# Performance work log

Hardware: AMD Instinct MI355X
Metric: run time of the kernel (lower is better)

The kernel has to match this reference:

```python
import jax, jax.numpy as jnp
import numpy as np

N = 50000   # nodes
E = 800000  # edges
D = 128     # input_dim
H = 128     # hidden_dim
C = 40      # output_dim (classes)


def setup_inputs() -> dict:
    key = jax.random.key(0)
    ks = jax.random.split(key, 8)
    x = jax.random.normal(ks[0], (N, D), dtype=jnp.float32)
    edge_index = jax.random.randint(ks[1], (2, E), 0, N, dtype=jnp.int32)
    sD = 1.0 / np.sqrt(D)
    sH = 1.0 / np.sqrt(H)
    W1 = jax.random.uniform(ks[2], (D, H), jnp.float32, -sD, sD)
    b1 = jnp.zeros((H,), jnp.float32)
    W2 = jax.random.uniform(ks[3], (H, H), jnp.float32, -sH, sH)
    b2 = jnp.zeros((H,), jnp.float32)
    W3 = jax.random.uniform(ks[4], (H, C), jnp.float32, -sH, sH)
    b3 = jnp.zeros((C,), jnp.float32)
    return {"x": x, "edge_index": edge_index,
            "W1": W1, "b1": b1, "W2": W2, "b2": b2, "W3": W3, "b3": b3}


def reference(x, edge_index, W1, b1, W2, b2, W3, b3):
    # GCNConv: out = D^{-1/2} (A + I) D^{-1/2} (x @ W) + b
    src = edge_index[0]
    dst = edge_index[1]
    loop = jnp.arange(N, dtype=src.dtype)
    src_f = jnp.concatenate([src, loop])  # [E+N] with self-loops
    dst_f = jnp.concatenate([dst, loop])
    deg = jax.ops.segment_sum(jnp.ones(E + N, x.dtype), dst_f, num_segments=N)
    dinv = jax.lax.rsqrt(jnp.maximum(deg, 1.0))  # deg >= 1 due to self-loops
    norm = dinv[src_f] * dinv[dst_f]  # [E+N]

    def conv(h, W, b):
        h = h @ W                       # [N, F_out]
        msg = h[src_f] * norm[:, None]  # [E+N, F_out] gathered messages
        return jax.ops.segment_sum(msg, dst_f, num_segments=N) + b

    h = jax.nn.relu(conv(x, W1, b1))
    h = jax.nn.relu(conv(h, W2, b2))  # dropout is identity in eval mode
    return conv(h, W3, b3)
```

## Files before the change

### kernel.cpp

```cpp
#include <hip/hip_runtime.h>

typedef unsigned short ushort_t;
typedef unsigned int uint_t;


__global__ __launch_bounds__(256) void k_scan(
        const int* __restrict__ deg, unsigned long long* __restrict__ partials,
        int* __restrict__ rowptr, int* __restrict__ cursor,
        float* __restrict__ dinv, int n) {
    __shared__ int s[256];
    __shared__ int sprefix;
    const int b = blockIdx.x, t = threadIdx.x;
    const int i = b * 256 + t;
    int v = (i < n) ? deg[i] : 0;
    s[t] = v;
    __syncthreads();
    for (int off = 1; off < 256; off <<= 1) {
        int u = (t >= off) ? s[t - off] : 0;
        __syncthreads();
        s[t] += u;
        __syncthreads();
    }
    if (t == 0) {
        __hip_atomic_store(&partials[b],
                ((unsigned long long)s[255] << 2) | 1ull,
                __ATOMIC_RELEASE, __HIP_MEMORY_SCOPE_AGENT);
        if (b == 0) {
            __hip_atomic_store(&partials[0],
                    ((unsigned long long)s[255] << 2) | 2ull,
                    __ATOMIC_RELEASE, __HIP_MEMORY_SCOPE_AGENT);
            sprefix = 0;
        }
    }
    if (b > 0 && t < 64) {
        int acc = 0;
        int k = b - 1;
        for (;;) {
            int idx = k - t;
            unsigned long long p;
            unsigned st;
            do {
                if (idx >= 0) {
                    p = __hip_atomic_load(&partials[idx],
                            __ATOMIC_ACQUIRE, __HIP_MEMORY_SCOPE_AGENT);
                } else {
                    p = 2ull;
                }
                st = (unsigned)(p & 3ull);
            } while (st == 0);
            unsigned long long bal = __ballot(st == 2);
            int L = (bal != 0) ? (__ffsll((unsigned long long)bal) - 1) : 64;
            int val = (int)(p >> 2);
            int contrib = (t <= L) ? val : 0;
            #pragma unroll
            for (int o = 32; o > 0; o >>= 1) contrib += __shfl_down(contrib, o);
            if (t == 0) acc += contrib;
            if (L < 64) break;
            k -= 64;
        }
        if (t == 0) {
            __hip_atomic_store(&partials[b],
                    (((unsigned long long)(acc + s[255])) << 2) | 2ull,
                    __ATOMIC_RELEASE, __HIP_MEMORY_SCOPE_AGENT);
            sprefix = acc;
        }
    }
    __syncthreads();
    if (i < n) {
        int ex = sprefix + s[t] - v;
        rowptr[i] = ex;
        cursor[i] = ex;
        dinv[i] = rsqrtf((float)(v + 1));
        if (i == n - 1) rowptr[n] = ex + v;
    }
}

__global__ __launch_bounds__(256) void k_fill(const int* __restrict__ ei,
                                              int* __restrict__ cursor,
                                              const float* __restrict__ dinv,
                                              int2* __restrict__ csr, int E, int n) {
    const int xcd = blockIdx.x & 7;
    const int e = (blockIdx.x >> 3) * 256 + threadIdx.x;
    if (e >= E) return;
    int d = ei[E + e];
    const int lo = (int)(((long long)xcd * n) >> 3);
    const int hi = (int)(((long long)(xcd + 1) * n) >> 3);
    if (d < lo || d >= hi) return;
    int s = ei[e];
    int pos = atomicAdd(&cursor[d], 1);
    int2 p;
    p.x = s;
    p.y = __float_as_int(dinv[s] * dinv[d]);
    csr[pos] = p;
}

__device__ __forceinline__ ushort_t f2bf_rne(float f) {
    uint_t u = __float_as_uint(f);
    u += 0x7fffu + ((u >> 16) & 1u);
    return (ushort_t)(u >> 16);
}
__device__ __forceinline__ float bflo(uint_t u) {
    return __uint_as_float(u << 16);
}
__device__ __forceinline__ float bfhi(uint_t u) {
    return __uint_as_float(u & 0xffff0000u);
}

__global__ __launch_bounds__(256) void k_l1(const float* __restrict__ X,
                                            const float* __restrict__ W,
                                            ushort_t* __restrict__ Y, int N,
                                            const int* __restrict__ ei,
                                            int* __restrict__ deg, int E,
                                            int gemmGrid) {
    __shared__ float sX[32][132];
    __shared__ float sW[32][128];
    if ((int)blockIdx.x >= gemmGrid) {
        int e = ((int)blockIdx.x - gemmGrid) * 256 + threadIdx.x;
        if (e < E) atomicAdd(&deg[ei[E + e]], 1);
        return;
    }
    const int tid = threadIdx.x;
    const int bm = blockIdx.x * 128;
    const int m0 = (tid >> 4) * 8;
    const int c4 = (tid & 15) * 4;
    const int xf = tid & 7;
    float acc[8][8] = {};
    for (int k0 = 0; k0 < 128; k0 += 32) {
        #pragma unroll
        for (int it = 0; it < 4; ++it) {
            int i = tid + it * 256;
            int row = bm + (i >> 3);
            int rc = min(row, N - 1);
            float4 v = *(const float4*)(X + (size_t)rc * 128 + k0 + xf * 4);
            int m = i >> 3;
            sX[xf * 4 + 0][m] = v.x;
            sX[xf * 4 + 1][m] = v.y;
            sX[xf * 4 + 2][m] = v.z;
            sX[xf * 4 + 3][m] = v.w;
        }
        #pragma unroll
        for (int it = 0; it < 4; ++it) {
            int i = tid + it * 256;
            int wr = i >> 5;
            int wf = i & 31;
            *(float4*)(&sW[wr][wf * 4]) =
                *(const float4*)(W + (size_t)(k0 + wr) * 128 + wf * 4);
        }
        __syncthreads();
        #pragma unroll
        for (int kk = 0; kk < 32; ++kk) {
            float4 a0 = *(const float4*)(&sX[kk][m0]);
            float4 a1 = *(const float4*)(&sX[kk][m0 + 4]);
            float4 b0 = *(const float4*)(&sW[kk][c4]);
            float4 b1 = *(const float4*)(&sW[kk][64 + c4]);
            float av[8] = {a0.x, a0.y, a0.z, a0.w, a1.x, a1.y, a1.z, a1.w};
            float bv[8] = {b0.x, b0.y, b0.z, b0.w, b1.x, b1.y, b1.z, b1.w};
            #pragma unroll
            for (int r = 0; r < 8; ++r)
                #pragma unroll
                for (int c = 0; c < 8; ++c)
                    acc[r][c] = fmaf(av[r], bv[c], acc[r][c]);
        }
        __syncthreads();
    }
    #pragma unroll
    for (int r = 0; r < 8; ++r) {
        int row = bm + m0 + r;
        if (row < N) {
            ushort4 o0 = {f2bf_rne(acc[r][0]), f2bf_rne(acc[r][1]),
                          f2bf_rne(acc[r][2]), f2bf_rne(acc[r][3])};
            ushort4 o1 = {f2bf_rne(acc[r][4]), f2bf_rne(acc[r][5]),
                          f2bf_rne(acc[r][6]), f2bf_rne(acc[r][7])};
            *(ushort4*)(Y + (size_t)row * 128 + c4)      = o0;
            *(ushort4*)(Y + (size_t)row * 128 + 64 + c4) = o1;
        }
    }
}

__global__ __launch_bounds__(256) void k_gemm128(const float* __restrict__ X,
                                                 const float* __restrict__ W,
                                                 ushort_t* __restrict__ Y, int N) {
    __shared__ float sX[32][132];
    __shared__ float sW[32][128];
    const int tid = threadIdx.x;
    const int bm = blockIdx.x * 128;
    const int m0 = (tid >> 4) * 8;
    const int c4 = (tid & 15) * 4;
    const int xf = tid & 7;
    float acc[8][8] = {};
    for (int k0 = 0; k0 < 128; k0 += 32) {
        #pragma unroll
        for (int it = 0; it < 4; ++it) {
            int i = tid + it * 256;
            int row = bm + (i >> 3);
            int rc = min(row, N - 1);
            float4 v = *(const float4*)(X + (size_t)rc * 128 + k0 + xf * 4);
            int m = i >> 3;
            sX[xf * 4 + 0][m] = v.x;
            sX[xf * 4 + 1][m] = v.y;
            sX[xf * 4 + 2][m] = v.z;
            sX[xf * 4 + 3][m] = v.w;
        }
        #pragma unroll
        for (int it = 0; it < 4; ++it) {
            int i = tid + it * 256;
            int wr = i >> 5;
            int wf = i & 31;
            *(float4*)(&sW[wr][wf * 4]) =
                *(const float4*)(W + (size_t)(k0 + wr) * 128 + wf * 4);
        }
        __syncthreads();
        #pragma unroll
        for (int kk = 0; kk < 32; ++kk) {
            float4 a0 = *(const float4*)(&sX[kk][m0]);
            float4 a1 = *(const float4*)(&sX[kk][m0 + 4]);
            float4 b0 = *(const float4*)(&sW[kk][c4]);
            float4 b1 = *(const float4*)(&sW[kk][64 + c4]);
            float av[8] = {a0.x, a0.y, a0.z, a0.w, a1.x, a1.y, a1.z, a1.w};
            float bv[8] = {b0.x, b0.y, b0.z, b0.w, b1.x, b1.y, b1.z, b1.w};
            #pragma unroll
            for (int r = 0; r < 8; ++r)
                #pragma unroll
                for (int c = 0; c < 8; ++c)
                    acc[r][c] = fmaf(av[r], bv[c], acc[r][c]);
        }
        __syncthreads();
    }
    #pragma unroll
    for (int r = 0; r < 8; ++r) {
        int row = bm + m0 + r;
        if (row < N) {
            ushort4 o0 = {f2bf_rne(acc[r][0]), f2bf_rne(acc[r][1]),
                          f2bf_rne(acc[r][2]), f2bf_rne(acc[r][3])};
            ushort4 o1 = {f2bf_rne(acc[r][4]), f2bf_rne(acc[r][5]),
                          f2bf_rne(acc[r][6]), f2bf_rne(acc[r][7])};
            *(ushort4*)(Y + (size_t)row * 128 + c4)      = o0;
            *(ushort4*)(Y + (size_t)row * 128 + 64 + c4) = o1;
        }
    }
}

__global__ __launch_bounds__(256) void k_gemm40(const float* __restrict__ X,
                                                const float* __restrict__ W,
                                                ushort_t* __restrict__ Y, int N) {
    __shared__ float sX[32][132];
    __shared__ float sW[32][40];
    const int tid = threadIdx.x;
    const int bm = blockIdx.x * 128;
    const int m0 = (tid >> 3) * 4;
    const int n0 = (tid & 7) * 5;
    const int xf = tid & 7;
    float acc[4][5] = {};
    for (int k0 = 0; k0 < 128; k0 += 32) {
        #pragma unroll
        for (int it = 0; it < 4; ++it) {
            int i = tid + it * 256;
            int row = bm + (i >> 3);
            int rc = min(row, N - 1);
            float4 v = *(const float4*)(X + (size_t)rc * 128 + k0 + xf * 4);
            int m = i >> 3;
            sX[xf * 4 + 0][m] = v.x;
            sX[xf * 4 + 1][m] = v.y;
            sX[xf * 4 + 2][m] = v.z;
            sX[xf * 4 + 3][m] = v.w;
        }
        for (int i = tid; i < 320; i += 256) {
            int wr = i / 10;
            int wf = i - wr * 10;
            *(float4*)(&sW[wr][wf * 4]) =
                *(const float4*)(W + (size_t)(k0 + wr) * 40 + wf * 4);
        }
        __syncthreads();
        #pragma unroll
        for (int kk = 0; kk < 32; ++kk) {
            float4 a = *(const float4*)(&sX[kk][m0]);
            float av[4] = {a.x, a.y, a.z, a.w};
            #pragma unroll
            for (int c = 0; c < 5; ++c) {
                float b = sW[kk][n0 + c];
                #pragma unroll
                for (int r = 0; r < 4; ++r)
                    acc[r][c] = fmaf(av[r], b, acc[r][c]);
            }
        }
        __syncthreads();
    }
    #pragma unroll
    for (int r = 0; r < 4; ++r) {
        int row = bm + m0 + r;
        if (row < N) {
            #pragma unroll
            for (int c = 0; c < 5; ++c)
                Y[(size_t)row * 64 + n0 + c] = f2bf_rne(acc[r][c]);
        }
    }
}

template <bool RELU>
__global__ __launch_bounds__(256) void k_agg128(
        const ushort_t* __restrict__ XW, const int* __restrict__ rowptr,
        const int2* __restrict__ csr, const float* __restrict__ dinv,
        const float* __restrict__ bias, float* __restrict__ out, int n) {
    const int lane = threadIdx.x & 63;
    const int wv = __builtin_amdgcn_readfirstlane(threadIdx.x >> 6);
    const int d = blockIdx.x * 4 + wv;
    if (d >= n) return;
    const uint_t* xw = (const uint_t*)XW;
    float dv = dinv[d];
    float w0 = dv * dv;
    uint_t sq = xw[(size_t)d * 64 + lane];
    float2 a;
    a.x = w0 * bflo(sq);
    a.y = w0 * bfhi(sq);
    int j = rowptr[d], end = rowptr[d + 1];
    for (; j + 8 <= end; j += 8) {
        int2 p0 = csr[j + 0], p1 = csr[j + 1], p2 = csr[j + 2], p3 = csr[j + 3];
        int2 p4 = csr[j + 4], p5 = csr[j + 5], p6 = csr[j + 6], p7 = csr[j + 7];
        uint_t u0 = xw[(size_t)p0.x * 64 + lane];
        uint_t u1 = xw[(size_t)p1.x * 64 + lane];
        uint_t u2 = xw[(size_t)p2.x * 64 + lane];
        uint_t u3 = xw[(size_t)p3.x * 64 + lane];
        uint_t u4 = xw[(size_t)p4.x * 64 + lane];
        uint_t u5 = xw[(size_t)p5.x * 64 + lane];
        uint_t u6 = xw[(size_t)p6.x * 64 + lane];
        uint_t u7 = xw[(size_t)p7.x * 64 + lane];
        float w0e = __int_as_float(p0.y), w1e = __int_as_float(p1.y);
        float w2e = __int_as_float(p2.y), w3e = __int_as_float(p3.y);
        float w4e = __int_as_float(p4.y), w5e = __int_as_float(p5.y);
        float w6e = __int_as_float(p6.y), w7e = __int_as_float(p7.y);
        a.x = fmaf(w0e, bflo(u0), a.x); a.y = fmaf(w0e, bfhi(u0), a.y);
        a.x = fmaf(w1e, bflo(u1), a.x); a.y = fmaf(w1e, bfhi(u1), a.y);
        a.x = fmaf(w2e, bflo(u2), a.x); a.y = fmaf(w2e, bfhi(u2), a.y);
        a.x = fmaf(w3e, bflo(u3), a.x); a.y = fmaf(w3e, bfhi(u3), a.y);
        a.x = fmaf(w4e, bflo(u4), a.x); a.y = fmaf(w4e, bfhi(u4), a.y);
        a.x = fmaf(w5e, bflo(u5), a.x); a.y = fmaf(w5e, bfhi(u5), a.y);
        a.x = fmaf(w6e, bflo(u6), a.x); a.y = fmaf(w6e, bfhi(u6), a.y);
        a.x = fmaf(w7e, bflo(u7), a.x); a.y = fmaf(w7e, bfhi(u7), a.y);
    }
    for (; j < end; ++j) {
        int2 p = csr[j];
        float we = __int_as_float(p.y);
        uint_t u = xw[(size_t)p.x * 64 + lane];
        a.x = fmaf(we, bflo(u), a.x);
        a.y = fmaf(we, bfhi(u), a.y);
    }
    float2 b = ((const float2*)bias)[lane];
    a.x += b.x; a.y += b.y;
    if (RELU) {
        a.x = fmaxf(a.x, 0.f);
        a.y = fmaxf(a.y, 0.f);
    }
    ((float2*)out)[(size_t)d * 64 + lane] = a;
}

__global__ __launch_bounds__(256) void k_agg40(
        const ushort_t* __restrict__ XW, const int* __restrict__ rowptr,
        const int2* __restrict__ csr, const float* __restrict__ dinv,
        const float* __restrict__ bias, float* __restrict__ out, int n) {
    const int lane = threadIdx.x & 31;
    const int sub  = threadIdx.x >> 5;
    const int d = blockIdx.x * 8 + sub;
    if (d >= n || lane >= 20) return;
    const uint_t* xw = (const uint_t*)XW;
    float dv = dinv[d];
    float w0 = dv * dv;
    uint_t sq = xw[(size_t)d * 32 + lane];
    float2 a;
    a.x = w0 * bflo(sq);
    a.y = w0 * bfhi(sq);
    int j = rowptr[d], end = rowptr[d + 1];
    for (; j + 4 <= end; j += 4) {
        int2 p0 = csr[j + 0], p1 = csr[j + 1], p2 = csr[j + 2], p3 = csr[j + 3];
        uint_t u0 = xw[(size_t)p0.x * 32 + lane];
        uint_t u1 = xw[(size_t)p1.x * 32 + lane];
        uint_t u2 = xw[(size_t)p2.x * 32 + lane];
        uint_t u3 = xw[(size_t)p3.x * 32 + lane];
        float w0e = __int_as_float(p0.y), w1e = __int_as_float(p1.y);
        float w2e = __int_as_float(p2.y), w3e = __int_as_float(p3.y);
        a.x = fmaf(w0e, bflo(u0), a.x); a.y = fmaf(w0e, bfhi(u0), a.y);
        a.x = fmaf(w1e, bflo(u1), a.x); a.y = fmaf(w1e, bfhi(u1), a.y);
        a.x = fmaf(w2e, bflo(u2), a.x); a.y = fmaf(w2e, bfhi(u2), a.y);
        a.x = fmaf(w3e, bflo(u3), a.x); a.y = fmaf(w3e, bfhi(u3), a.y);
    }
    for (; j < end; ++j) {
        int2 p = csr[j];
        float we = __int_as_float(p.y);
        uint_t u = xw[(size_t)p.x * 32 + lane];
        a.x = fmaf(we, bflo(u), a.x);
        a.y = fmaf(we, bfhi(u), a.y);
    }
    float2 b = ((const float2*)bias)[lane];
    a.x += b.x; a.y += b.y;
    ((float2*)out)[(size_t)d * 20 + lane] = a;
}

static inline int cdiv(long long a, int b) { return (int)((a + b - 1) / b); }

extern "C" void kernel_launch(void* const* d_in, const int* in_sizes, int n_in,
                              void* d_out, int out_size, void* d_ws, size_t ws_size,
                              hipStream_t stream) {
    const float* x  = (const float*)d_in[0];
    const int*   ei = (const int*)d_in[1];
    const float* W1 = (const float*)d_in[2];
    const float* b1 = (const float*)d_in[3];
    const float* W2 = (const float*)d_in[4];
    const float* b2 = (const float*)d_in[5];
    const float* W3 = (const float*)d_in[6];
    const float* b3 = (const float*)d_in[7];
    float* out = (float*)d_out;

    const int N = in_sizes[0] / 128;
    const int E = in_sizes[1] / 2;
    const int nb = cdiv(N, 256);

    char* ws = (char*)d_ws;
    int*   deg    = (int*)ws;                 ws += (size_t)N * 4;
    unsigned long long* partials = (unsigned long long*)ws;
                                              ws += (size_t)nb * 8;
    int*   rowptr = (int*)ws;                 ws += (size_t)(N + 1) * 4;
    int*   cursor = (int*)ws;                 ws += (size_t)N * 4;
    float* dinv   = (float*)ws;               ws += (size_t)N * 4;
    ws = (char*)(((uintptr_t)ws + 127) & ~(uintptr_t)127);
    int2*  csr    = (int2*)ws;                ws += (size_t)E * 8;
    char*  bufA   = ws;                       ws += (size_t)N * 128 * 4;
    float* bufB   = (float*)ws;

    const int BT = 256;
    const int gemmGrid = cdiv(N, 128);
    const int degGrid  = cdiv(E, BT);

    hipMemsetAsync(deg, 0, (size_t)N * 4 + (size_t)nb * 8, stream);

    k_l1<<<gemmGrid + degGrid, 256, 0, stream>>>(x, W1, (ushort_t*)bufA, N,
                                                 ei, deg, E, gemmGrid);
    k_scan<<<nb, 256, 0, stream>>>(deg, partials, rowptr, cursor, dinv, N);
    k_fill<<<cdiv(E, BT) * 8, 256, 0, stream>>>(ei, cursor, dinv, csr, E, N);

    k_agg128<true><<<cdiv(N, 4), 256, 0, stream>>>((const ushort_t*)bufA, rowptr, csr, dinv, b1, bufB, N);
    k_gemm128<<<cdiv(N, 128), 256, 0, stream>>>(bufB, W2, (ushort_t*)bufA, N);
    k_agg128<true><<<cdiv(N, 4), 256, 0, stream>>>((const ushort_t*)bufA, rowptr, csr, dinv, b2, bufB, N);
    k_gemm40<<<cdiv(N, 128), 256, 0, stream>>>(bufB, W3, (ushort_t*)bufA, N);
    k_agg40<<<cdiv(N, 8), 256, 0, stream>>>((const ushort_t*)bufA, rowptr, csr, dinv, b3, out, N);
}
```

Before: 301.6 us.

## Fuse neighbor aggregation with following dense GEMM via shared-memory tile

Each block now aggregates 64 destination rows (bias+ReLU) into shared memory and immediately multiplies the tile by the next layer's weight matrix, emitting bf16 output. This removes the fp32 intermediate buffer write/read between aggregation and GEMM and drops two kernel launches. In exchange, each wave serially processes 16 nodes, so there are fewer waves in flight to hide gather latency, and the shared-memory tile (~33KB for the 128-wide case) lowers occupancy; the GEMM also uses smaller per-thread tiles and strided LDS reads.

```diff
diff --git a/kernel.cpp b/kernel.cpp
--- a/kernel.cpp
+++ b/kernel.cpp
@@ -177,30 +177,71 @@
     }
 }
 
-__global__ __launch_bounds__(256) void k_gemm128(const float* __restrict__ X,
-                                                 const float* __restrict__ W,
-                                                 ushort_t* __restrict__ Y, int N) {
-    __shared__ float sX[32][132];
+__global__ __launch_bounds__(256) void k_ag128(
+        const ushort_t* __restrict__ XW, const int* __restrict__ rowptr,
+        const int2* __restrict__ csr, const float* __restrict__ dinv,
+        const float* __restrict__ bias, const float* __restrict__ W,
+        ushort_t* __restrict__ Y, int n) {
+    __shared__ float sA[64][130];
     __shared__ float sW[32][128];
     const int tid = threadIdx.x;
-    const int bm = blockIdx.x * 128;
-    const int m0 = (tid >> 4) * 8;
+    const int lane = tid & 63;
+    const int wv = __builtin_amdgcn_readfirstlane(tid >> 6);
+    const int bm = blockIdx.x * 64;
+    const uint_t* xw = (const uint_t*)XW;
+    #pragma unroll 1
+    for (int mi = 0; mi < 16; ++mi) {
+        const int m = wv * 16 + mi;
+        const int d = bm + m;
+        if (d >= n) break;
+        float dv = dinv[d];
+        float w0 = dv * dv;
+        uint_t sq = xw[(size_t)d * 64 + lane];
+        float2 a;
+        a.x = w0 * bflo(sq);
+        a.y = w0 * bfhi(sq);
+        int j = rowptr[d], end = rowptr[d + 1];
+        for (; j + 8 <= end; j += 8) {
+            int2 p0 = csr[j + 0], p1 = csr[j + 1], p2 = csr[j + 2], p3 = csr[j + 3];
+            int2 p4 = csr[j + 4], p5 = csr[j + 5], p6 = csr[j + 6], p7 = csr[j + 7];
+            uint_t u0 = xw[(size_t)p0.x * 64 + lane];
+            uint_t u1 = xw[(size_t)p1.x * 64 + lane];
+            uint_t u2 = xw[(size_t)p2.x * 64 + lane];
+            uint_t u3 = xw[(size_t)p3.x * 64 + lane];
+            uint_t u4 = xw[(size_t)p4.x * 64 + lane];
+            uint_t u5 = xw[(size_t)p5.x * 64 + lane];
+            uint_t u6 = xw[(size_t)p6.x * 64 + lane];
+            uint_t u7 = xw[(size_t)p7.x * 64 + lane];
+            float w0e = __int_as_float(p0.y), w1e = __int_as_float(p1.y);
+            float w2e = __int_as_float(p2.y), w3e = __int_as_float(p3.y);
+            float w4e = __int_as_float(p4.y), w5e = __int_as_float(p5.y);
+            float w6e = __int_as_float(p6.y), w7e = __int_as_float(p7.y);
+            a.x = fmaf(w0e, bflo(u0), a.x); a.y = fmaf(w0e, bfhi(u0), a.y);
+            a.x = fmaf(w1e, bflo(u1), a.x); a.y = fmaf(w1e, bfhi(u1), a.y);
+            a.x = fmaf(w2e, bflo(u2), a.x); a.y = fmaf(w2e, bfhi(u2), a.y);
+            a.x = fmaf(w3e, bflo(u3), a.x); a.y = fmaf(w3e, bfhi(u3), a.y);
+            a.x = fmaf(w4e, bflo(u4), a.x); a.y = fmaf(w4e, bfhi(u4), a.y);
+            a.x = fmaf(w5e, bflo(u5), a.x); a.y = fmaf(w5e, bfhi(u5), a.y);
+            a.x = fmaf(w6e, bflo(u6), a.x); a.y = fmaf(w6e, bfhi(u6), a.y);
+            a.x = fmaf(w7e, bflo(u7), a.x); a.y = fmaf(w7e, bfhi(u7), a.y);
+        }
+        for (; j < end; ++j) {
+            int2 p = csr[j];
+            float we = __int_as_float(p.y);
+            uint_t u = xw[(size_t)p.x * 64 + lane];
+            a.x = fmaf(we, bflo(u), a.x);
+            a.y = fmaf(we, bfhi(u), a.y);
+        }
+        float2 b = ((const float2*)bias)[lane];
+        a.x = fmaxf(a.x + b.x, 0.f);
+        a.y = fmaxf(a.y + b.y, 0.f);
+        *(float2*)(&sA[m][lane * 2]) = a;
+    }
+    __syncthreads();
+    const int m0 = (tid >> 4) * 4;
     const int c4 = (tid & 15) * 4;
-    const int xf = tid & 7;
-    float acc[8][8] = {};
+    float acc[4][8] = {};
     for (int k0 = 0; k0 < 128; k0 += 32) {
-        #pragma unroll
-        for (int it = 0; it < 4; ++it) {
-            int i = tid + it * 256;
-            int row = bm + (i >> 3);
-            int rc = min(row, N - 1);
-            float4 v = *(const float4*)(X + (size_t)rc * 128 + k0 + xf * 4);
-            int m = i >> 3;
-            sX[xf * 4 + 0][m] = v.x;
-            sX[xf * 4 + 1][m] = v.y;
-            sX[xf * 4 + 2][m] = v.z;
-            sX[xf * 4 + 3][m] = v.w;
-        }
         #pragma unroll
         for (int it = 0; it < 4; ++it) {
             int i = tid + it * 256;
@@ -212,14 +253,14 @@
         __syncthreads();
         #pragma unroll
         for (int kk = 0; kk < 32; ++kk) {
-            float4 a0 = *(const float4*)(&sX[kk][m0]);
-            float4 a1 = *(const float4*)(&sX[kk][m0 + 4]);
+            float av[4];
+            #pragma unroll
+            for (int r = 0; r < 4; ++r) av[r] = sA[m0 + r][k0 + kk];
             float4 b0 = *(const float4*)(&sW[kk][c4]);
             float4 b1 = *(const float4*)(&sW[kk][64 + c4]);
-            float av[8] = {a0.x, a0.y, a0.z, a0.w, a1.x, a1.y, a1.z, a1.w};
             float bv[8] = {b0.x, b0.y, b0.z, b0.w, b1.x, b1.y, b1.z, b1.w};
             #pragma unroll
-            for (int r = 0; r < 8; ++r)
+            for (int r = 0; r < 4; ++r)
                 #pragma unroll
                 for (int c = 0; c < 8; ++c)
                     acc[r][c] = fmaf(av[r], bv[c], acc[r][c]);
@@ -227,9 +268,9 @@
         __syncthreads();
     }
     #pragma unroll
-    for (int r = 0; r < 8; ++r) {
+    for (int r = 0; r < 4; ++r) {
         int row = bm + m0 + r;
-        if (row < N) {
+        if (row < n) {
             ushort4 o0 = {f2bf_rne(acc[r][0]), f2bf_rne(acc[r][1]),
                           f2bf_rne(acc[r][2]), f2bf_rne(acc[r][3])};
             ushort4 o1 = {f2bf_rne(acc[r][4]), f2bf_rne(acc[r][5]),
@@ -240,30 +281,71 @@
     }
 }
 
-__global__ __launch_bounds__(256) void k_gemm40(const float* __restrict__ X,
-                                                const float* __restrict__ W,
-                                                ushort_t* __restrict__ Y, int N) {
-    __shared__ float sX[32][132];
+__global__ __launch_bounds__(256) void k_ag40(
+        const ushort_t* __restrict__ XW, const int* __restrict__ rowptr,
+        const int2* __restrict__ csr, const float* __restrict__ dinv,
+        const float* __restrict__ bias, const float* __restrict__ W,
+        ushort_t* __restrict__ Y, int n) {
+    __shared__ float sA[64][130];
     __shared__ float sW[32][40];
     const int tid = threadIdx.x;
-    const int bm = blockIdx.x * 128;
-    const int m0 = (tid >> 3) * 4;
+    const int lane = tid & 63;
+    const int wv = __builtin_amdgcn_readfirstlane(tid >> 6);
+    const int bm = blockIdx.x * 64;
+    const uint_t* xw = (const uint_t*)XW;
+    #pragma unroll 1
+    for (int mi = 0; mi < 16; ++mi) {
+        const int m = wv * 16 + mi;
+        const int d = bm + m;
+        if (d >= n) break;
+        float dv = dinv[d];
+        float w0 = dv * dv;
+        uint_t sq = xw[(size_t)d * 64 + lane];
+        float2 a;
+        a.x = w0 * bflo(sq);
+        a.y = w0 * bfhi(sq);
+        int j = rowptr[d], end = rowptr[d + 1];
+        for (; j + 8 <= end; j += 8) {
+            int2 p0 = csr[j + 0], p1 = csr[j + 1], p2 = csr[j + 2], p3 = csr[j + 3];
+            int2 p4 = csr[j + 4], p5 = csr[j + 5], p6 = csr[j + 6], p7 = csr[j + 7];
+            uint_t u0 = xw[(size_t)p0.x * 64 + lane];
+            uint_t u1 = xw[(size_t)p1.x * 64 + lane];
+            uint_t u2 = xw[(size_t)p2.x * 64 + lane];
+            uint_t u3 = xw[(size_t)p3.x * 64 + lane];
+            uint_t u4 = xw[(size_t)p4.x * 64 + lane];
+            uint_t u5 = xw[(size_t)p5.x * 64 + lane];
+            uint_t u6 = xw[(size_t)p6.x * 64 + lane];
+            uint_t u7 = xw[(size_t)p7.x * 64 + lane];
+            float w0e = __int_as_float(p0.y), w1e = __int_as_float(p1.y);
+            float w2e = __int_as_float(p2.y), w3e = __int_as_float(p3.y);
+            float w4e = __int_as_float(p4.y), w5e = __int_as_float(p5.y);
+            float w6e = __int_as_float(p6.y), w7e = __int_as_float(p7.y);
+            a.x = fmaf(w0e, bflo(u0), a.x); a.y = fmaf(w0e, bfhi(u0), a.y);
+            a.x = fmaf(w1e, bflo(u1), a.x); a.y = fmaf(w1e, bfhi(u1), a.y);
+            a.x = fmaf(w2e, bflo(u2), a.x); a.y = fmaf(w2e, bfhi(u2), a.y);
+            a.x = fmaf(w3e, bflo(u3), a.x); a.y = fmaf(w3e, bfhi(u3), a.y);
+            a.x = fmaf(w4e, bflo(u4), a.x); a.y = fmaf(w4e, bfhi(u4), a.y);
+            a.x = fmaf(w5e, bflo(u5), a.x); a.y = fmaf(w5e, bfhi(u5), a.y);
+            a.x = fmaf(w6e, bflo(u6), a.x); a.y = fmaf(w6e, bfhi(u6), a.y);
+            a.x = fmaf(w7e, bflo(u7), a.x); a.y = fmaf(w7e, bfhi(u7), a.y);
+        }
+        for (; j < end; ++j) {
+            int2 p = csr[j];
+            float we = __int_as_float(p.y);
+            uint_t u = xw[(size_t)p.x * 64 + lane];
+            a.x = fmaf(we, bflo(u), a.x);
+            a.y = fmaf(we, bfhi(u), a.y);
+        }
+        float2 b = ((const float2*)bias)[lane];
+        a.x = fmaxf(a.x + b.x, 0.f);
+        a.y = fmaxf(a.y + b.y, 0.f);
+        *(float2*)(&sA[m][lane * 2]) = a;
+    }
+    __syncthreads();
+    const int m0 = (tid >> 3) * 2;
     const int n0 = (tid & 7) * 5;
-    const int xf = tid & 7;
-    float acc[4][5] = {};
+    float acc[2][5] = {};
     for (int k0 = 0; k0 < 128; k0 += 32) {
-        #pragma unroll
-        for (int it = 0; it < 4; ++it) {
-            int i = tid + it * 256;
-            int row = bm + (i >> 3);
-            int rc = min(row, N - 1);
-            float4 v = *(const float4*)(X + (size_t)rc * 128 + k0 + xf * 4);
-            int m = i >> 3;
-            sX[xf * 4 + 0][m] = v.x;
-            sX[xf * 4 + 1][m] = v.y;
-            sX[xf * 4 + 2][m] = v.z;
-            sX[xf * 4 + 3][m] = v.w;
-        }
         for (int i = tid; i < 320; i += 256) {
             int wr = i / 10;
             int wf = i - wr * 10;
@@ -273,84 +355,26 @@
         __syncthreads();
         #pragma unroll
         for (int kk = 0; kk < 32; ++kk) {
-            float4 a = *(const float4*)(&sX[kk][m0]);
-            float av[4] = {a.x, a.y, a.z, a.w};
+            float av0 = sA[m0][k0 + kk];
+            float av1 = sA[m0 + 1][k0 + kk];
             #pragma unroll
             for (int c = 0; c < 5; ++c) {
                 float b = sW[kk][n0 + c];
-                #pragma unroll
-                for (int r = 0; r < 4; ++r)
-                    acc[r][c] = fmaf(av[r], b, acc[r][c]);
+                acc[0][c] = fmaf(av0, b, acc[0][c]);
+                acc[1][c] = fmaf(av1, b, acc[1][c]);
             }
         }
         __syncthreads();
     }
     #pragma unroll
-    for (int r = 0; r < 4; ++r) {
+    for (int r = 0; r < 2; ++r) {
         int row = bm + m0 + r;
-        if (row < N) {
+        if (row < n) {
             #pragma unroll
             for (int c = 0; c < 5; ++c)
                 Y[(size_t)row * 64 + n0 + c] = f2bf_rne(acc[r][c]);
         }
     }
-}
-
-template <bool RELU>
-__global__ __launch_bounds__(256) void k_agg128(
-        const ushort_t* __restrict__ XW, const int* __restrict__ rowptr,
-        const int2* __restrict__ csr, const float* __restrict__ dinv,
-        const float* __restrict__ bias, float* __restrict__ out, int n) {
-    const int lane = threadIdx.x & 63;
-    const int wv = __builtin_amdgcn_readfirstlane(threadIdx.x >> 6);
-    const int d = blockIdx.x * 4 + wv;
-    if (d >= n) return;
-    const uint_t* xw = (const uint_t*)XW;
-    float dv = dinv[d];
-    float w0 = dv * dv;
-    uint_t sq = xw[(size_t)d * 64 + lane];
-    float2 a;
-    a.x = w0 * bflo(sq);
-    a.y = w0 * bfhi(sq);
-    int j = rowptr[d], end = rowptr[d + 1];
-    for (; j + 8 <= end; j += 8) {
-        int2 p0 = csr[j + 0], p1 = csr[j + 1], p2 = csr[j + 2], p3 = csr[j + 3];
-        int2 p4 = csr[j + 4], p5 = csr[j + 5], p6 = csr[j + 6], p7 = csr[j + 7];
-        uint_t u0 = xw[(size_t)p0.x * 64 + lane];
-        uint_t u1 = xw[(size_t)p1.x * 64 + lane];
-        uint_t u2 = xw[(size_t)p2.x * 64 + lane];
-        uint_t u3 = xw[(size_t)p3.x * 64 + lane];
-        uint_t u4 = xw[(size_t)p4.x * 64 + lane];
-        uint_t u5 = xw[(size_t)p5.x * 64 + lane];
-        uint_t u6 = xw[(size_t)p6.x * 64 + lane];
-        uint_t u7 = xw[(size_t)p7.x * 64 + lane];
-        float w0e = __int_as_float(p0.y), w1e = __int_as_float(p1.y);
-        float w2e = __int_as_float(p2.y), w3e = __int_as_float(p3.y);
-        float w4e = __int_as_float(p4.y), w5e = __int_as_float(p5.y);
-        float w6e = __int_as_float(p6.y), w7e = __int_as_float(p7.y);
-        a.x = fmaf(w0e, bflo(u0), a.x); a.y = fmaf(w0e, bfhi(u0), a.y);
-        a.x = fmaf(w1e, bflo(u1), a.x); a.y = fmaf(w1e, bfhi(u1), a.y);
-        a.x = fmaf(w2e, bflo(u2), a.x); a.y = fmaf(w2e, bfhi(u2), a.y);
-        a.x = fmaf(w3e, bflo(u3), a.x); a.y = fmaf(w3e, bfhi(u3), a.y);
-        a.x = fmaf(w4e, bflo(u4), a.x); a.y = fmaf(w4e, bfhi(u4), a.y);
-        a.x = fmaf(w5e, bflo(u5), a.x); a.y = fmaf(w5e, bfhi(u5), a.y);
-        a.x = fmaf(w6e, bflo(u6), a.x); a.y = fmaf(w6e, bfhi(u6), a.y);
-        a.x = fmaf(w7e, bflo(u7), a.x); a.y = fmaf(w7e, bfhi(u7), a.y);
-    }
-    for (; j < end; ++j) {
-        int2 p = csr[j];
-        float we = __int_as_float(p.y);
-        uint_t u = xw[(size_t)p.x * 64 + lane];
-        a.x = fmaf(we, bflo(u), a.x);
-        a.y = fmaf(we, bfhi(u), a.y);
-    }
-    float2 b = ((const float2*)bias)[lane];
-    a.x += b.x; a.y += b.y;
-    if (RELU) {
-        a.x = fmaxf(a.x, 0.f);
-        a.y = fmaxf(a.y, 0.f);
-    }
-    ((float2*)out)[(size_t)d * 64 + lane] = a;
 }
 
 __global__ __launch_bounds__(256) void k_agg40(
@@ -421,9 +445,10 @@
     int*   cursor = (int*)ws;                 ws += (size_t)N * 4;
     float* dinv   = (float*)ws;               ws += (size_t)N * 4;
     ws = (char*)(((uintptr_t)ws + 127) & ~(uintptr_t)127);
-    int2*  csr    = (int2*)ws;                ws += (size_t)E * 8;
-    char*  bufA   = ws;                       ws += (size_t)N * 128 * 4;
-    float* bufB   = (float*)ws;
+    int2*     csr  = (int2*)ws;               ws += (size_t)E * 8;
+    ushort_t* bufA = (ushort_t*)ws;           ws += (size_t)N * 128 * 2;
+    ushort_t* bufC = (ushort_t*)ws;           ws += (size_t)N * 128 * 2;
+    ushort_t* bufD = (ushort_t*)ws;
 
     const int BT = 256;
     const int gemmGrid = cdiv(N, 128);
@@ -431,14 +456,12 @@
 
     hipMemsetAsync(deg, 0, (size_t)N * 4 + (size_t)nb * 8, stream);
 
-    k_l1<<<gemmGrid + degGrid, 256, 0, stream>>>(x, W1, (ushort_t*)bufA, N,
+    k_l1<<<gemmGrid + degGrid, 256, 0, stream>>>(x, W1, bufA, N,
                                                  ei, deg, E, gemmGrid);
     k_scan<<<nb, 256, 0, stream>>>(deg, partials, rowptr, cursor, dinv, N);
     k_fill<<<cdiv(E, BT) * 8, 256, 0, stream>>>(ei, cursor, dinv, csr, E, N);
 
-    k_agg128<true><<<cdiv(N, 4), 256, 0, stream>>>((const ushort_t*)bufA, rowptr, csr, dinv, b1, bufB, N);
-    k_gemm128<<<cdiv(N, 128), 256, 0, stream>>>(bufB, W2, (ushort_t*)bufA, N);
-    k_agg128<true><<<cdiv(N, 4), 256, 0, stream>>>((const ushort_t*)bufA, rowptr, csr, dinv, b2, bufB, N);
-    k_gemm40<<<cdiv(N, 128), 256, 0, stream>>>(bufB, W3, (ushort_t*)bufA, N);
-    k_agg40<<<cdiv(N, 8), 256, 0, stream>>>((const ushort_t*)bufA, rowptr, csr, dinv, b3, out, N);
-}
+    k_ag128<<<cdiv(N, 64), 256, 0, stream>>>(bufA, rowptr, csr, dinv, b1, W2, bufC, N);
+    k_ag40 <<<cdiv(N, 64), 256, 0, stream>>>(bufC, rowptr, csr, dinv, b2, W3, bufD, N);
+    k_agg40<<<cdiv(N, 8), 256, 0, stream>>>(bufD, rowptr, csr, dinv, b3, out, N);
+}
```

After: 373.5 us. 23.8% more time.

## Store source-only CSR and recompute edge weights from dinv during aggregation

Applied to the files above, without the earlier changes.

The CSR entries shrink from (src, weight) pairs to source indices only. Aggregation kernels now compute each edge weight as dinv[src]*dinv[dst] on the fly. The fill kernel handles four edges per thread with a vector load of destinations and uses nontemporal loads for the streamed edge and CSR arrays. This halves CSR write and read traffic across three aggregation passes, at the cost of an extra random gather into dinv per edge, though that array is small enough to stay cache resident.

```diff
diff --git a/kernel.cpp b/kernel.cpp
--- a/kernel.cpp
+++ b/kernel.cpp
@@ -2,6 +2,7 @@
 
 typedef unsigned short ushort_t;
 typedef unsigned int uint_t;
+typedef int int4v __attribute__((ext_vector_type(4)));
 
 
 __global__ __launch_bounds__(256) void k_scan(
@@ -77,21 +78,33 @@
 
 __global__ __launch_bounds__(256) void k_fill(const int* __restrict__ ei,
                                               int* __restrict__ cursor,
-                                              const float* __restrict__ dinv,
-                                              int2* __restrict__ csr, int E, int n) {
+                                              int* __restrict__ csr, int E, int n) {
     const int xcd = blockIdx.x & 7;
-    const int e = (blockIdx.x >> 3) * 256 + threadIdx.x;
-    if (e >= E) return;
-    int d = ei[E + e];
+    const int e4 = (((blockIdx.x >> 3) * 256 + threadIdx.x) << 2);
+    if (e4 >= E) return;
     const int lo = (int)(((long long)xcd * n) >> 3);
     const int hi = (int)(((long long)(xcd + 1) * n) >> 3);
-    if (d < lo || d >= hi) return;
-    int s = ei[e];
-    int pos = atomicAdd(&cursor[d], 1);
-    int2 p;
-    p.x = s;
-    p.y = __float_as_int(dinv[s] * dinv[d]);
-    csr[pos] = p;
+    if (e4 + 4 <= E) {
+        int4v d4 = __builtin_nontemporal_load((const int4v*)(ei + E + e4));
+        #pragma unroll
+        for (int k = 0; k < 4; ++k) {
+            int d = d4[k];
+            if (d >= lo && d < hi) {
+                int s = __builtin_nontemporal_load(ei + e4 + k);
+                int pos = atomicAdd(&cursor[d], 1);
+                csr[pos] = s;
+            }
+        }
+    } else {
+        for (int k = 0; k < 4 && e4 + k < E; ++k) {
+            int d = __builtin_nontemporal_load(ei + E + e4 + k);
+            if (d >= lo && d < hi) {
+                int s = __builtin_nontemporal_load(ei + e4 + k);
+                int pos = atomicAdd(&cursor[d], 1);
+                csr[pos] = s;
+            }
+        }
+    }
 }
 
 __device__ __forceinline__ ushort_t f2bf_rne(float f) {
@@ -116,7 +129,7 @@
     __shared__ float sW[32][128];
     if ((int)blockIdx.x >= gemmGrid) {
         int e = ((int)blockIdx.x - gemmGrid) * 256 + threadIdx.x;
-        if (e < E) atomicAdd(&deg[ei[E + e]], 1);
+        if (e < E) atomicAdd(&deg[__builtin_nontemporal_load(ei + E + e)], 1);
         return;
     }
     const int tid = threadIdx.x;
@@ -299,7 +312,7 @@
 template <bool RELU>
 __global__ __launch_bounds__(256) void k_agg128(
         const ushort_t* __restrict__ XW, const int* __restrict__ rowptr,
-        const int2* __restrict__ csr, const float* __restrict__ dinv,
+        const int* __restrict__ csr, const float* __restrict__ dinv,
         const float* __restrict__ bias, float* __restrict__ out, int n) {
     const int lane = threadIdx.x & 63;
     const int wv = __builtin_amdgcn_readfirstlane(threadIdx.x >> 6);
@@ -314,20 +327,26 @@
     a.y = w0 * bfhi(sq);
     int j = rowptr[d], end = rowptr[d + 1];
     for (; j + 8 <= end; j += 8) {
-        int2 p0 = csr[j + 0], p1 = csr[j + 1], p2 = csr[j + 2], p3 = csr[j + 3];
-        int2 p4 = csr[j + 4], p5 = csr[j + 5], p6 = csr[j + 6], p7 = csr[j + 7];
-        uint_t u0 = xw[(size_t)p0.x * 64 + lane];
-        uint_t u1 = xw[(size_t)p1.x * 64 + lane];
-        uint_t u2 = xw[(size_t)p2.x * 64 + lane];
-        uint_t u3 = xw[(size_t)p3.x * 64 + lane];
-        uint_t u4 = xw[(size_t)p4.x * 64 + lane];
-        uint_t u5 = xw[(size_t)p5.x * 64 + lane];
-        uint_t u6 = xw[(size_t)p6.x * 64 + lane];
-        uint_t u7 = xw[(size_t)p7.x * 64 + lane];
-        float w0e = __int_as_float(p0.y), w1e = __int_as_float(p1.y);
-        float w2e = __int_as_float(p2.y), w3e = __int_as_float(p3.y);
-        float w4e = __int_as_float(p4.y), w5e = __int_as_float(p5.y);
-        float w6e = __int_as_float(p6.y), w7e = __int_as_float(p7.y);
+        int s0 = __builtin_nontemporal_load(csr + j + 0);
+        int s1 = __builtin_nontemporal_load(csr + j + 1);
+        int s2 = __builtin_nontemporal_load(csr + j + 2);
+        int s3 = __builtin_nontemporal_load(csr + j + 3);
+        int s4 = __builtin_nontemporal_load(csr + j + 4);
+        int s5 = __builtin_nontemporal_load(csr + j + 5);
+        int s6 = __builtin_nontemporal_load(csr + j + 6);
+        int s7 = __builtin_nontemporal_load(csr + j + 7);
+        uint_t u0 = xw[(size_t)s0 * 64 + lane];
+        uint_t u1 = xw[(size_t)s1 * 64 + lane];
+        uint_t u2 = xw[(size_t)s2 * 64 + lane];
+        uint_t u3 = xw[(size_t)s3 * 64 + lane];
+        uint_t u4 = xw[(size_t)s4 * 64 + lane];
+        uint_t u5 = xw[(size_t)s5 * 64 + lane];
+        uint_t u6 = xw[(size_t)s6 * 64 + lane];
+        uint_t u7 = xw[(size_t)s7 * 64 + lane];
+        float w0e = dinv[s0] * dv, w1e = dinv[s1] * dv;
+        float w2e = dinv[s2] * dv, w3e = dinv[s3] * dv;
+        float w4e = dinv[s4] * dv, w5e = dinv[s5] * dv;
+        float w6e = dinv[s6] * dv, w7e = dinv[s7] * dv;
         a.x = fmaf(w0e, bflo(u0), a.x); a.y = fmaf(w0e, bfhi(u0), a.y);
         a.x = fmaf(w1e, bflo(u1), a.x); a.y = fmaf(w1e, bfhi(u1), a.y);
         a.x = fmaf(w2e, bflo(u2), a.x); a.y = fmaf(w2e, bfhi(u2), a.y);
@@ -338,9 +357,9 @@
         a.x = fmaf(w7e, bflo(u7), a.x); a.y = fmaf(w7e, bfhi(u7), a.y);
     }
     for (; j < end; ++j) {
-        int2 p = csr[j];
-        float we = __int_as_float(p.y);
-        uint_t u = xw[(size_t)p.x * 64 + lane];
+        int s = __builtin_nontemporal_load(csr + j);
+        float we = dinv[s] * dv;
+        uint_t u = xw[(size_t)s * 64 + lane];
         a.x = fmaf(we, bflo(u), a.x);
         a.y = fmaf(we, bfhi(u), a.y);
     }
@@ -355,7 +374,7 @@
 
 __global__ __launch_bounds__(256) void k_agg40(
         const ushort_t* __restrict__ XW, const int* __restrict__ rowptr,
-        const int2* __restrict__ csr, const float* __restrict__ dinv,
+        const int* __restrict__ csr, const float* __restrict__ dinv,
         const float* __restrict__ bias, float* __restrict__ out, int n) {
     const int lane = threadIdx.x & 31;
     const int sub  = threadIdx.x >> 5;
@@ -370,22 +389,25 @@
     a.y = w0 * bfhi(sq);
     int j = rowptr[d], end = rowptr[d + 1];
     for (; j + 4 <= end; j += 4) {
-        int2 p0 = csr[j + 0], p1 = csr[j + 1], p2 = csr[j + 2], p3 = csr[j + 3];
-        uint_t u0 = xw[(size_t)p0.x * 32 + lane];
-        uint_t u1 = xw[(size_t)p1.x * 32 + lane];
-        uint_t u2 = xw[(size_t)p2.x * 32 + lane];
-        uint_t u3 = xw[(size_t)p3.x * 32 + lane];
-        float w0e = __int_as_float(p0.y), w1e = __int_as_float(p1.y);
-        float w2e = __int_as_float(p2.y), w3e = __int_as_float(p3.y);
+        int s0 = __builtin_nontemporal_load(csr + j + 0);
+        int s1 = __builtin_nontemporal_load(csr + j + 1);
+        int s2 = __builtin_nontemporal_load(csr + j + 2);
+        int s3 = __builtin_nontemporal_load(csr + j + 3);
+        uint_t u0 = xw[(size_t)s0 * 32 + lane];
+        uint_t u1 = xw[(size_t)s1 * 32 + lane];
+        uint_t u2 = xw[(size_t)s2 * 32 + lane];
+        uint_t u3 = xw[(size_t)s3 * 32 + lane];
+        float w0e = dinv[s0] * dv, w1e = dinv[s1] * dv;
+        float w2e = dinv[s2] * dv, w3e = dinv[s3] * dv;
         a.x = fmaf(w0e, bflo(u0), a.x); a.y = fmaf(w0e, bfhi(u0), a.y);
         a.x = fmaf(w1e, bflo(u1), a.x); a.y = fmaf(w1e, bfhi(u1), a.y);
         a.x = fmaf(w2e, bflo(u2), a.x); a.y = fmaf(w2e, bfhi(u2), a.y);
         a.x = fmaf(w3e, bflo(u3), a.x); a.y = fmaf(w3e, bfhi(u3), a.y);
     }
     for (; j < end; ++j) {
-        int2 p = csr[j];
-        float we = __int_as_float(p.y);
-        uint_t u = xw[(size_t)p.x * 32 + lane];
+        int s = __builtin_nontemporal_load(csr + j);
+        float we = dinv[s] * dv;
+        uint_t u = xw[(size_t)s * 32 + lane];
         a.x = fmaf(we, bflo(u), a.x);
         a.y = fmaf(we, bfhi(u), a.y);
     }
@@ -421,7 +443,8 @@
     int*   cursor = (int*)ws;                 ws += (size_t)N * 4;
     float* dinv   = (float*)ws;               ws += (size_t)N * 4;
     ws = (char*)(((uintptr_t)ws + 127) & ~(uintptr_t)127);
-    int2*  csr    = (int2*)ws;                ws += (size_t)E * 8;
+    int*   csr    = (int*)ws;                 ws += (size_t)E * 4;
+    ws = (char*)(((uintptr_t)ws + 127) & ~(uintptr_t)127);
     char*  bufA   = ws;                       ws += (size_t)N * 128 * 4;
     float* bufB   = (float*)ws;
 
@@ -434,7 +457,7 @@
     k_l1<<<gemmGrid + degGrid, 256, 0, stream>>>(x, W1, (ushort_t*)bufA, N,
                                                  ei, deg, E, gemmGrid);
     k_scan<<<nb, 256, 0, stream>>>(deg, partials, rowptr, cursor, dinv, N);
-    k_fill<<<cdiv(E, BT) * 8, 256, 0, stream>>>(ei, cursor, dinv, csr, E, N);
+    k_fill<<<cdiv(E, BT * 4) * 8, 256, 0, stream>>>(ei, cursor, csr, E, N);
 
     k_agg128<true><<<cdiv(N, 4), 256, 0, stream>>>((const ushort_t*)bufA, rowptr, csr, dinv, b1, bufB, N);
     k_gemm128<<<cdiv(N, 128), 256, 0, stream>>>(bufB, W2, (ushort_t*)bufA, N);
```

After: 312.4 us. 3.6% more time.
